# Kernel tuning notes

Hardware: AMD Instinct MI355X
Metric: run time of the kernel (lower is better)

## Reference

```python
import jax, jax.numpy as jnp
import numpy as np

B, P, N, L, H = 8, 1024, 32, 125, 256
E = 3 + L  # embed_dim = 3 local coords + latent_dim
OUTPUT_BIAS = 0.5   # cfg.supervision != 'sdf'
LEVEL_SET = -0.07   # cfg.level_set
SOFT_SCALE = 100.0  # cfg.soft_transfer_scale


def setup_inputs() -> dict:
    key = jax.random.key(0)
    ks = jax.random.split(key, 12)
    rn = lambda k, s, sc=1.0: jax.random.normal(k, s, dtype=jnp.float32) * sc
    X = rn(ks[0], (B, P, 3))
    latents = rn(ks[1], (N, B, L))
    constants = jax.random.uniform(ks[2], (B, N), minval=0.5, maxval=1.5, dtype=jnp.float32)
    scales = jax.random.uniform(ks[3], (B, N, 3), minval=0.5, maxval=1.5, dtype=jnp.float32)
    rotations = rn(ks[4], (B, N, 3, 3))
    centers = rn(ks[5], (B, N, 3))
    W0 = rn(ks[6], (N, E, H), 1.0 / np.sqrt(E))
    W1 = rn(ks[7], (N, H, H), 1.0 / np.sqrt(H))
    W2 = rn(ks[8], (N, H, H), 1.0 / np.sqrt(H))
    Wout = rn(ks[9], (N, H, 1), 1.0 / np.sqrt(H))
    return dict(X=X, latents=latents, constants=constants, scales=scales,
                rotations=rotations, centers=centers,
                W0=W0, b0=jnp.zeros((N, H), jnp.float32),
                W1=W1, b1=jnp.zeros((N, H), jnp.float32),
                W2=W2, b2=jnp.zeros((N, H), jnp.float32),
                Wout=Wout, bout=jnp.zeros((N, 1), jnp.float32),
                use_constants=1)


def _forward(X, latents, constants, scales, rotations, centers,
             W0, b0, W1, b1, W2, b2, Wout, bout, use_constants):
    b, p, _ = X.shape
    n, _, l = latents.shape
    # global_to_local: rotate (X - center) into each node frame, divide by scale
    diff = X[:, :, None, :] - centers[:, None]                      # [B,P,N,3]
    local = jnp.einsum('bnij,bpnj->bpni', rotations, diff) / scales[:, None]
    # concat local coords with per-node latent broadcast over points
    lat = jnp.broadcast_to(latents.transpose(1, 0, 2)[:, None], (b, p, n, l))
    inp = jnp.concatenate([local, lat], axis=-1)                    # [B,P,N,E]
    # per-node MLP stack as batched (grouped) GEMMs over the node axis
    h = jax.nn.relu(jnp.einsum('bpne,neh->bpnh', inp, W0) + b0)
    h = jax.nn.relu(jnp.einsum('bpnh,nhk->bpnk', h, W1) + b1)
    h = jax.nn.relu(jnp.einsum('bpnh,nhk->bpnk', h, W2) + b2)
    pred_sdf = jnp.einsum('bpnh,nho->bpno', h, Wout) + bout + OUTPUT_BIAS  # [B,P,N,1]
    # sample_rbf_weights: anisotropic gaussian weight per node
    w = jnp.exp(-0.5 * jnp.sum(local * local, axis=-1))             # [B,P,N]
    if use_constants:
        w = w * constants[:, None, :]
    w = w[..., None]                                                # [B,P,N,1]
    weighted_points_sdf = w * pred_sdf
    ldif_values = jnp.sum(weighted_points_sdf, axis=2)              # [B,P,1]
    # compute_inverse_occupancy: sigmoid(soft_scale * (level_set - values))
    class_pred = jax.nn.sigmoid(SOFT_SCALE * (LEVEL_SET - ldif_values))
    return ldif_values, class_pred


def reference(X, latents, constants, scales, rotations, centers,
              W0, b0, W1, b1, W2, b2, Wout, bout, use_constants):
    return _forward(X, latents, constants, scales, rotations, centers,
                    W0, b0, W1, b1, W2, b2, Wout, bout, use_constants)
```

## Files before the change

### kernel.cpp

```cpp
#include <hip/hip_runtime.h>
#include <math.h>

#define B_ 8
#define P_ 1024
#define N_ 32
#define L_ 125
#define H_ 256
#define E_ 128
#define MT 64

static_assert(E_ == 3 + L_, "embed dim mismatch");

typedef _Float16 half8 __attribute__((ext_vector_type(8)));
typedef _Float16 half4v __attribute__((ext_vector_type(4)));
typedef float f32x16 __attribute__((ext_vector_type(16)));

__global__ void prep(const float* __restrict__ latents,
                     const float* __restrict__ W0,
                     const float* __restrict__ b0,
                     const float* __restrict__ W1,
                     const float* __restrict__ W2,
                     float* __restrict__ Z,
                     _Float16* __restrict__ WThi,
                     _Float16* __restrict__ WTlo) {
  const int bid = blockIdx.x;
  const int t = threadIdx.x;
  if (bid < N_ * B_) {
    __shared__ float lat[L_];
    const int n = bid >> 3, b = bid & 7;
    if (t < L_) lat[t] = latents[(n * B_ + b) * L_ + t];
    __syncthreads();
    const float* w0 = W0 + ((size_t)n * E_ + 3) * H_ + t;
    float acc = b0[n * H_ + t];
#pragma unroll 5
    for (int l = 0; l < L_; ++l)
      acc = fmaf(lat[l], w0[(size_t)l * H_], acc);
    Z[(b * N_ + n) * H_ + t] = acc;
  } else {
    const int id = bid - N_ * B_;
    const int node = id >> 5;
    const int layer = (id >> 4) & 1;
    const int jb = (id >> 2) & 3;
    const int kb = id & 3;
    const float* W = (layer == 0 ? W1 : W2) + (size_t)node * H_ * H_;
    _Float16* dhi = WThi + ((size_t)layer * N_ + node) * H_ * H_;
    _Float16* dlo = WTlo + ((size_t)layer * N_ + node) * H_ * H_;
    __shared__ float tile[64][65];
    {
      const int col = t & 63;
#pragma unroll
      for (int i = 0; i < 16; ++i) {
        const int row = (t >> 6) * 16 + i;
        tile[row][col] = W[(size_t)(kb * 64 + row) * H_ + jb * 64 + col];
      }
    }
    __syncthreads();
    const int j_l = t >> 2;
    const int j = jb * 64 + j_l;
    const int w = j >> 5, lc = j & 31;
    const int kq = (t & 3) * 16;
    const int kc = kb * 4 + (t & 3);
    half8 hv0, hv1, lv0, lv1;
#pragma unroll
    for (int q = 0; q < 16; ++q) {
      const float v = tile[kq + q][j_l];
      const _Float16 hh = (_Float16)v;
      const _Float16 ll = (_Float16)(v - (float)hh);
      if (q < 8) { hv0[q] = hh; lv0[q] = ll; }
      else       { hv1[q - 8] = hh; lv1[q - 8] = ll; }
    }
    const size_t o0 = (size_t)w * 8192 + (size_t)kc * 512 + lc * 8;
    const size_t o1 = o0 + 256;
    *(half8*)(dhi + o0) = hv0;
    *(half8*)(dhi + o1) = hv1;
    *(half8*)(dlo + o0) = lv0;
    *(half8*)(dlo + o1) = lv1;
  }
}

__global__ __launch_bounds__(512, 2)
void mlp_main(const float* __restrict__ X,
              const float* __restrict__ constants,
              const float* __restrict__ scales,
              const float* __restrict__ rotations,
              const float* __restrict__ centers,
              const float* __restrict__ W0,
              const float* __restrict__ b1,
              const float* __restrict__ b2,
              const float* __restrict__ Wout,
              const float* __restrict__ bout,
              const float* __restrict__ Z,
              const _Float16* __restrict__ WThi,
              const _Float16* __restrict__ WTlo,
              const int* __restrict__ use_constants,
              float* __restrict__ pred) {
  __shared__ _Float16 h_hi[MT * H_];
  __shared__ _Float16 h_lo[MT * H_];
  __shared__ float loc[MT][3];
  __shared__ float wgt[MT];
  __shared__ float predpart[MT];

  const int ell = blockIdx.x;
  const int node = (ell & 7) * 4 + ((ell >> 3) & 3);
  const int p0 = (ell >> 5) * MT;
  const int b = p0 >> 10;
  const int tid = threadIdx.x;
  const int lane = tid & 63;
  const int w = tid >> 6;
  const int lc = lane & 31;
  const int kh = lane >> 5;

  if (tid < MT) {
    predpart[tid] = 0.f;
    const int pidx = p0 + tid;
    const float x0 = X[pidx * 3 + 0];
    const float x1 = X[pidx * 3 + 1];
    const float x2 = X[pidx * 3 + 2];
    const float* R = rotations + (size_t)(b * N_ + node) * 9;
    const float* C = centers + (size_t)(b * N_ + node) * 3;
    const float* S = scales + (size_t)(b * N_ + node) * 3;
    const float d0 = x0 - C[0], d1 = x1 - C[1], d2 = x2 - C[2];
    const float l0 = (R[0] * d0 + R[1] * d1 + R[2] * d2) / S[0];
    const float l1 = (R[3] * d0 + R[4] * d1 + R[5] * d2) / S[1];
    const float l2 = (R[6] * d0 + R[7] * d1 + R[8] * d2) / S[2];
    loc[tid][0] = l0; loc[tid][1] = l1; loc[tid][2] = l2;
    float ww = expf(-0.5f * (l0 * l0 + l1 * l1 + l2 * l2));
    if (use_constants[0] != 0) ww *= constants[b * N_ + node];
    wgt[tid] = ww;
  }
  __syncthreads();

  {
    const int m = lane;
    const float l0 = loc[m][0], l1 = loc[m][1], l2 = loc[m][2];
    const float* w0p = W0 + (size_t)node * E_ * H_;
    const float* zp = Z + (size_t)(b * N_ + node) * H_;
    char* hhp = (char*)h_hi + m * 512;
    char* hlp = (char*)h_lo + m * 512;
    const int mx = m & 31;
#pragma unroll
    for (int j = w * 32; j < w * 32 + 32; j += 4) {
      const float4 a0 = *(const float4*)(w0p + j);
      const float4 a1 = *(const float4*)(w0p + H_ + j);
      const float4 a2 = *(const float4*)(w0p + 2 * H_ + j);
      const float4 zz = *(const float4*)(zp + j);
      float v[4];
      v[0] = fmaxf(fmaf(l2, a2.x, fmaf(l1, a1.x, fmaf(l0, a0.x, zz.x))), 0.f);
      v[1] = fmaxf(fmaf(l2, a2.y, fmaf(l1, a1.y, fmaf(l0, a0.y, zz.y))), 0.f);
      v[2] = fmaxf(fmaf(l2, a2.z, fmaf(l1, a1.z, fmaf(l0, a0.z, zz.z))), 0.f);
      v[3] = fmaxf(fmaf(l2, a2.w, fmaf(l1, a1.w, fmaf(l0, a0.w, zz.w))), 0.f);
      half4v hv, lv;
#pragma unroll
      for (int r = 0; r < 4; ++r) {
        const _Float16 h16 = (_Float16)v[r];
        hv[r] = h16;
        lv[r] = (_Float16)(v[r] - (float)h16);
      }
      const int off = (((j >> 3) ^ mx) << 4) + ((j & 7) << 1);
      *(half4v*)(hhp + off) = hv;
      *(half4v*)(hlp + off) = lv;
    }
  }
  __syncthreads();

  f32x16 acc0, acc1;

  const size_t wb = (size_t)node * H_ * H_ + (size_t)w * 8192 + (kh * 32 + lc) * 8;
  const _Float16* wt1hi = WThi + wb;
  const _Float16* wt1lo = WTlo + wb;
  const _Float16* wt2hi = WThi + (size_t)N_ * H_ * H_ + wb;
  const _Float16* wt2lo = WTlo + (size_t)N_ * H_ * H_ + wb;

  const char* rbh0 = (const char*)h_hi + lc * 512;
  const char* rbh1 = (const char*)h_hi + (32 + lc) * 512;
  const char* rbl0 = (const char*)h_lo + lc * 512;
  const char* rbl1 = (const char*)h_lo + (32 + lc) * 512;

#define LDA(AH, AL, K) \
  AH = *(const half8*)(wh + (K) * 512); \
  AL = *(const half8*)(wl + (K) * 512);
#define LDB(B0, B1, B2, B3, K) { \
  const int so_ = ((2 * (K) + kh) ^ lc) << 4; \
  B0 = *(const half8*)(rbh0 + so_); \
  B1 = *(const half8*)(rbh1 + so_); \
  B2 = *(const half8*)(rbl0 + so_); \
  B3 = *(const half8*)(rbl1 + so_); }
#define MM(AH, AL, B0, B1, B2, B3) \
  __builtin_amdgcn_s_setprio(1); \
  acc0 = __builtin_amdgcn_mfma_f32_32x32x16_f16(AH, B0, acc0, 0, 0, 0); \
  acc1 = __builtin_amdgcn_mfma_f32_32x32x16_f16(AH, B1, acc1, 0, 0, 0); \
  acc0 = __builtin_amdgcn_mfma_f32_32x32x16_f16(AH, B2, acc0, 0, 0, 0); \
  acc1 = __builtin_amdgcn_mfma_f32_32x32x16_f16(AH, B3, acc1, 0, 0, 0); \
  acc0 = __builtin_amdgcn_mfma_f32_32x32x16_f16(AL, B0, acc0, 0, 0, 0); \
  acc1 = __builtin_amdgcn_mfma_f32_32x32x16_f16(AL, B1, acc1, 0, 0, 0); \
  __builtin_amdgcn_s_setprio(0);

  auto run_layer = [&](const _Float16* __restrict__ wh,
                       const _Float16* __restrict__ wl) {
    acc0 = (f32x16)(0.f);
    acc1 = (f32x16)(0.f);
    half8 A0H, A0L, A1H, A1L, A2H, A2L;
    half8 S0B0, S0B1, S0B2, S0B3, S1B0, S1B1, S1B2, S1B3;
    LDA(A0H, A0L, 0)
    LDA(A1H, A1L, 1)
    LDB(S0B0, S0B1, S0B2, S0B3, 0)
    LDA(A2H, A2L, 2)  LDB(S1B0, S1B1, S1B2, S1B3, 1)  MM(A0H, A0L, S0B0, S0B1, S0B2, S0B3)
    LDA(A0H, A0L, 3)  LDB(S0B0, S0B1, S0B2, S0B3, 2)  MM(A1H, A1L, S1B0, S1B1, S1B2, S1B3)
    LDA(A1H, A1L, 4)  LDB(S1B0, S1B1, S1B2, S1B3, 3)  MM(A2H, A2L, S0B0, S0B1, S0B2, S0B3)
    LDA(A2H, A2L, 5)  LDB(S0B0, S0B1, S0B2, S0B3, 4)  MM(A0H, A0L, S1B0, S1B1, S1B2, S1B3)
    LDA(A0H, A0L, 6)  LDB(S1B0, S1B1, S1B2, S1B3, 5)  MM(A1H, A1L, S0B0, S0B1, S0B2, S0B3)
    LDA(A1H, A1L, 7)  LDB(S0B0, S0B1, S0B2, S0B3, 6)  MM(A2H, A2L, S1B0, S1B1, S1B2, S1B3)
    LDA(A2H, A2L, 8)  LDB(S1B0, S1B1, S1B2, S1B3, 7)  MM(A0H, A0L, S0B0, S0B1, S0B2, S0B3)
    LDA(A0H, A0L, 9)  LDB(S0B0, S0B1, S0B2, S0B3, 8)  MM(A1H, A1L, S1B0, S1B1, S1B2, S1B3)
    LDA(A1H, A1L, 10) LDB(S1B0, S1B1, S1B2, S1B3, 9)  MM(A2H, A2L, S0B0, S0B1, S0B2, S0B3)
    LDA(A2H, A2L, 11) LDB(S0B0, S0B1, S0B2, S0B3, 10) MM(A0H, A0L, S1B0, S1B1, S1B2, S1B3)
    LDA(A0H, A0L, 12) LDB(S1B0, S1B1, S1B2, S1B3, 11) MM(A1H, A1L, S0B0, S0B1, S0B2, S0B3)
    LDA(A1H, A1L, 13) LDB(S0B0, S0B1, S0B2, S0B3, 12) MM(A2H, A2L, S1B0, S1B1, S1B2, S1B3)
    LDA(A2H, A2L, 14) LDB(S1B0, S1B1, S1B2, S1B3, 13) MM(A0H, A0L, S0B0, S0B1, S0B2, S0B3)
    LDA(A0H, A0L, 15) LDB(S0B0, S0B1, S0B2, S0B3, 14) MM(A1H, A1L, S1B0, S1B1, S1B2, S1B3)
                      LDB(S1B0, S1B1, S1B2, S1B3, 15) MM(A2H, A2L, S0B0, S0B1, S0B2, S0B3)
                                                      MM(A0H, A0L, S1B0, S1B1, S1B2, S1B3)
  };

  run_layer(wt1hi, wt1lo);
  __syncthreads();
  {
#pragma unroll
    for (int q = 0; q < 4; ++q) {
      const int jq = 32 * w + 8 * q + 4 * kh;
      const float4 bb = *(const float4*)(b1 + node * H_ + jq);
      const float bv[4] = {bb.x, bb.y, bb.z, bb.w};
      const int soff = ((((4 * w + q) ^ lc) << 4) + (kh << 3));
      half4v hv, lv;
#pragma unroll
      for (int r = 0; r < 4; ++r) {
        const float v = fmaxf(acc0[4 * q + r] + bv[r], 0.f);
        const _Float16 h16 = (_Float16)v;
        hv[r] = h16;
        lv[r] = (_Float16)(v - (float)h16);
      }
      *(half4v*)((char*)h_hi + lc * 512 + soff) = hv;
      *(half4v*)((char*)h_lo + lc * 512 + soff) = lv;
#pragma unroll
      for (int r = 0; r < 4; ++r) {
        const float v = fmaxf(acc1[4 * q + r] + bv[r], 0.f);
        const _Float16 h16 = (_Float16)v;
        hv[r] = h16;
        lv[r] = (_Float16)(v - (float)h16);
      }
      *(half4v*)((char*)h_hi + (32 + lc) * 512 + soff) = hv;
      *(half4v*)((char*)h_lo + (32 + lc) * 512 + soff) = lv;
    }
  }
  __syncthreads();

  run_layer(wt2hi, wt2lo);
  {
    float s0 = 0.f, s1 = 0.f;
#pragma unroll
    for (int q = 0; q < 4; ++q) {
      const int jq = 32 * w + 8 * q + 4 * kh;
      const float4 bb = *(const float4*)(b2 + node * H_ + jq);
      const float4 wo = *(const float4*)(Wout + node * H_ + jq);
      const float bv[4] = {bb.x, bb.y, bb.z, bb.w};
      const float wv[4] = {wo.x, wo.y, wo.z, wo.w};
#pragma unroll
      for (int r = 0; r < 4; ++r) {
        s0 = fmaf(fmaxf(acc0[4 * q + r] + bv[r], 0.f), wv[r], s0);
        s1 = fmaf(fmaxf(acc1[4 * q + r] + bv[r], 0.f), wv[r], s1);
      }
    }
    s0 += __shfl_xor(s0, 32, 64);
    s1 += __shfl_xor(s1, 32, 64);
    if (lane < 32) {
      atomicAdd(&predpart[lc], s0);
      atomicAdd(&predpart[32 + lc], s1);
    }
  }
  __syncthreads();

  if (tid < MT)
    pred[(size_t)node * (B_ * P_) + p0 + tid] =
        wgt[tid] * (predpart[tid] + bout[node] + 0.5f);
}

__global__ void finalize(const float* __restrict__ pred, float* __restrict__ out) {
  const int i = blockIdx.x * 256 + threadIdx.x;
  float v = 0.f;
#pragma unroll
  for (int n = 0; n < N_; ++n) v += pred[n * (B_ * P_) + i];
  out[i] = v;
  const float zz = 100.0f * (-0.07f - v);
  out[B_ * P_ + i] = 1.0f / (1.0f + expf(-zz));
}

extern "C" void kernel_launch(void* const* d_in, const int* in_sizes, int n_in,
                              void* d_out, int out_size, void* d_ws, size_t ws_size,
                              hipStream_t stream) {
  const float* X = (const float*)d_in[0];
  const float* latents = (const float*)d_in[1];
  const float* constants = (const float*)d_in[2];
  const float* scales = (const float*)d_in[3];
  const float* rotations = (const float*)d_in[4];
  const float* centers = (const float*)d_in[5];
  const float* W0 = (const float*)d_in[6];
  const float* b0 = (const float*)d_in[7];
  const float* W1 = (const float*)d_in[8];
  const float* b1 = (const float*)d_in[9];
  const float* W2 = (const float*)d_in[10];
  const float* b2 = (const float*)d_in[11];
  const float* Wout = (const float*)d_in[12];
  const float* bout = (const float*)d_in[13];
  const int* use_constants = (const int*)d_in[14];

  float* pred = (float*)d_ws;
  float* Zbuf = pred + (size_t)N_ * B_ * P_;
  _Float16* WThi = (_Float16*)(Zbuf + B_ * N_ * H_);
  _Float16* WTlo = WThi + (size_t)2 * N_ * H_ * H_;

  prep<<<dim3(N_ * B_ + N_ * 2 * 16), 256, 0, stream>>>(
      latents, W0, b0, W1, W2, Zbuf, WThi, WTlo);

  mlp_main<<<dim3(B_ * P_ / MT * N_), 512, 0, stream>>>(
      X, constants, scales, rotations, centers, W0, b1, b2, Wout, bout,
      Zbuf, WThi, WTlo, use_constants, pred);

  finalize<<<dim3(B_ * P_ / 256), 256, 0, stream>>>(pred, (float*)d_out);
}
```

Baseline: 322.7 us.

## Halve block to 4 waves, each computing two 32-column output tiles

The MLP kernel drops from 8 to 4 waves per block. Each wave now keeps four 32x32 accumulators and covers two column groups, so every B fragment read from LDS feeds twice as many MFMAs and LDS read traffic per FLOP goes down. The first-layer fill loop is widened so that 256 threads still cover all 64 rows by 256 columns. The cost is more accumulator and A-fragment registers per wave, plus a launch bound of 4 blocks per CU, which may limit occupancy or cause spills.

```diff
diff --git a/kernel.cpp b/kernel.cpp
--- a/kernel.cpp
+++ b/kernel.cpp
@@ -57,7 +57,7 @@
     __syncthreads();
     const int j_l = t >> 2;
     const int j = jb * 64 + j_l;
-    const int w = j >> 5, lc = j & 31;
+    const int jg = j >> 5, lc = j & 31;
     const int kq = (t & 3) * 16;
     const int kc = kb * 4 + (t & 3);
     half8 hv0, hv1, lv0, lv1;
@@ -69,7 +69,7 @@
       if (q < 8) { hv0[q] = hh; lv0[q] = ll; }
       else       { hv1[q - 8] = hh; lv1[q - 8] = ll; }
     }
-    const size_t o0 = (size_t)w * 8192 + (size_t)kc * 512 + lc * 8;
+    const size_t o0 = (size_t)jg * 8192 + (size_t)kc * 512 + lc * 8;
     const size_t o1 = o0 + 256;
     *(half8*)(dhi + o0) = hv0;
     *(half8*)(dhi + o1) = hv1;
@@ -78,7 +78,7 @@
   }
 }
 
-__global__ __launch_bounds__(512, 2)
+__global__ __launch_bounds__(256, 4)
 void mlp_main(const float* __restrict__ X,
               const float* __restrict__ constants,
               const float* __restrict__ scales,
@@ -131,7 +131,8 @@
   __syncthreads();
 
   {
-    const int m = lane;
+    const int m = tid & 63;
+    const int jr = (tid >> 6) * 64;
     const float l0 = loc[m][0], l1 = loc[m][1], l2 = loc[m][2];
     const float* w0p = W0 + (size_t)node * E_ * H_;
     const float* zp = Z + (size_t)(b * N_ + node) * H_;
@@ -139,7 +140,7 @@
     char* hlp = (char*)h_lo + m * 512;
     const int mx = m & 31;
 #pragma unroll
-    for (int j = w * 32; j < w * 32 + 32; j += 4) {
+    for (int j = jr; j < jr + 64; j += 4) {
       const float4 a0 = *(const float4*)(w0p + j);
       const float4 a1 = *(const float4*)(w0p + H_ + j);
       const float4 a2 = *(const float4*)(w0p + 2 * H_ + j);
@@ -163,9 +164,9 @@
   }
   __syncthreads();
 
-  f32x16 acc0, acc1;
-
-  const size_t wb = (size_t)node * H_ * H_ + (size_t)w * 8192 + (kh * 32 + lc) * 8;
+  f32x16 acc00, acc01, acc10, acc11;
+
+  const size_t wb = (size_t)node * H_ * H_ + (size_t)(2 * w) * 8192 + (kh * 32 + lc) * 8;
   const _Float16* wt1hi = WThi + wb;
   const _Float16* wt1lo = WTlo + wb;
   const _Float16* wt2hi = WThi + (size_t)N_ * H_ * H_ + wb;
@@ -176,80 +177,92 @@
   const char* rbl0 = (const char*)h_lo + lc * 512;
   const char* rbl1 = (const char*)h_lo + (32 + lc) * 512;
 
-#define LDA(AH, AL, K) \
-  AH = *(const half8*)(wh + (K) * 512); \
-  AL = *(const half8*)(wl + (K) * 512);
+#define LDA(H0, L0, H1, L1, K) \
+  H0 = *(const half8*)(wh + (K) * 512); \
+  L0 = *(const half8*)(wl + (K) * 512); \
+  H1 = *(const half8*)(wh + 8192 + (K) * 512); \
+  L1 = *(const half8*)(wl + 8192 + (K) * 512);
 #define LDB(B0, B1, B2, B3, K) { \
   const int so_ = ((2 * (K) + kh) ^ lc) << 4; \
   B0 = *(const half8*)(rbh0 + so_); \
   B1 = *(const half8*)(rbh1 + so_); \
   B2 = *(const half8*)(rbl0 + so_); \
   B3 = *(const half8*)(rbl1 + so_); }
-#define MM(AH, AL, B0, B1, B2, B3) \
+#define MM(H0, L0, H1, L1, B0, B1, B2, B3) \
   __builtin_amdgcn_s_setprio(1); \
-  acc0 = __builtin_amdgcn_mfma_f32_32x32x16_f16(AH, B0, acc0, 0, 0, 0); \
-  acc1 = __builtin_amdgcn_mfma_f32_32x32x16_f16(AH, B1, acc1, 0, 0, 0); \
-  acc0 = __builtin_amdgcn_mfma_f32_32x32x16_f16(AH, B2, acc0, 0, 0, 0); \
-  acc1 = __builtin_amdgcn_mfma_f32_32x32x16_f16(AH, B3, acc1, 0, 0, 0); \
-  acc0 = __builtin_amdgcn_mfma_f32_32x32x16_f16(AL, B0, acc0, 0, 0, 0); \
-  acc1 = __builtin_amdgcn_mfma_f32_32x32x16_f16(AL, B1, acc1, 0, 0, 0); \
+  acc00 = __builtin_amdgcn_mfma_f32_32x32x16_f16(H0, B0, acc00, 0, 0, 0); \
+  acc01 = __builtin_amdgcn_mfma_f32_32x32x16_f16(H0, B1, acc01, 0, 0, 0); \
+  acc10 = __builtin_amdgcn_mfma_f32_32x32x16_f16(H1, B0, acc10, 0, 0, 0); \
+  acc11 = __builtin_amdgcn_mfma_f32_32x32x16_f16(H1, B1, acc11, 0, 0, 0); \
+  acc00 = __builtin_amdgcn_mfma_f32_32x32x16_f16(H0, B2, acc00, 0, 0, 0); \
+  acc01 = __builtin_amdgcn_mfma_f32_32x32x16_f16(H0, B3, acc01, 0, 0, 0); \
+  acc10 = __builtin_amdgcn_mfma_f32_32x32x16_f16(H1, B2, acc10, 0, 0, 0); \
+  acc11 = __builtin_amdgcn_mfma_f32_32x32x16_f16(H1, B3, acc11, 0, 0, 0); \
+  acc00 = __builtin_amdgcn_mfma_f32_32x32x16_f16(L0, B0, acc00, 0, 0, 0); \
+  acc01 = __builtin_amdgcn_mfma_f32_32x32x16_f16(L0, B1, acc01, 0, 0, 0); \
+  acc10 = __builtin_amdgcn_mfma_f32_32x32x16_f16(L1, B0, acc10, 0, 0, 0); \
+  acc11 = __builtin_amdgcn_mfma_f32_32x32x16_f16(L1, B1, acc11, 0, 0, 0); \
   __builtin_amdgcn_s_setprio(0);
 
   auto run_layer = [&](const _Float16* __restrict__ wh,
                        const _Float16* __restrict__ wl) {
-    acc0 = (f32x16)(0.f);
-    acc1 = (f32x16)(0.f);
-    half8 A0H, A0L, A1H, A1L, A2H, A2L;
+    acc00 = (f32x16)(0.f);
+    acc01 = (f32x16)(0.f);
+    acc10 = (f32x16)(0.f);
+    acc11 = (f32x16)(0.f);
+    half8 A0H0, A0L0, A0H1, A0L1, A1H0, A1L0, A1H1, A1L1;
     half8 S0B0, S0B1, S0B2, S0B3, S1B0, S1B1, S1B2, S1B3;
-    LDA(A0H, A0L, 0)
-    LDA(A1H, A1L, 1)
+    LDA(A0H0, A0L0, A0H1, A0L1, 0)
     LDB(S0B0, S0B1, S0B2, S0B3, 0)
-    LDA(A2H, A2L, 2)  LDB(S1B0, S1B1, S1B2, S1B3, 1)  MM(A0H, A0L, S0B0, S0B1, S0B2, S0B3)
-    LDA(A0H, A0L, 3)  LDB(S0B0, S0B1, S0B2, S0B3, 2)  MM(A1H, A1L, S1B0, S1B1, S1B2, S1B3)
-    LDA(A1H, A1L, 4)  LDB(S1B0, S1B1, S1B2, S1B3, 3)  MM(A2H, A2L, S0B0, S0B1, S0B2, S0B3)
-    LDA(A2H, A2L, 5)  LDB(S0B0, S0B1, S0B2, S0B3, 4)  MM(A0H, A0L, S1B0, S1B1, S1B2, S1B3)
-    LDA(A0H, A0L, 6)  LDB(S1B0, S1B1, S1B2, S1B3, 5)  MM(A1H, A1L, S0B0, S0B1, S0B2, S0B3)
-    LDA(A1H, A1L, 7)  LDB(S0B0, S0B1, S0B2, S0B3, 6)  MM(A2H, A2L, S1B0, S1B1, S1B2, S1B3)
-    LDA(A2H, A2L, 8)  LDB(S1B0, S1B1, S1B2, S1B3, 7)  MM(A0H, A0L, S0B0, S0B1, S0B2, S0B3)
-    LDA(A0H, A0L, 9)  LDB(S0B0, S0B1, S0B2, S0B3, 8)  MM(A1H, A1L, S1B0, S1B1, S1B2, S1B3)
-    LDA(A1H, A1L, 10) LDB(S1B0, S1B1, S1B2, S1B3, 9)  MM(A2H, A2L, S0B0, S0B1, S0B2, S0B3)
-    LDA(A2H, A2L, 11) LDB(S0B0, S0B1, S0B2, S0B3, 10) MM(A0H, A0L, S1B0, S1B1, S1B2, S1B3)
-    LDA(A0H, A0L, 12) LDB(S1B0, S1B1, S1B2, S1B3, 11) MM(A1H, A1L, S0B0, S0B1, S0B2, S0B3)
-    LDA(A1H, A1L, 13) LDB(S0B0, S0B1, S0B2, S0B3, 12) MM(A2H, A2L, S1B0, S1B1, S1B2, S1B3)
-    LDA(A2H, A2L, 14) LDB(S1B0, S1B1, S1B2, S1B3, 13) MM(A0H, A0L, S0B0, S0B1, S0B2, S0B3)
-    LDA(A0H, A0L, 15) LDB(S0B0, S0B1, S0B2, S0B3, 14) MM(A1H, A1L, S1B0, S1B1, S1B2, S1B3)
-                      LDB(S1B0, S1B1, S1B2, S1B3, 15) MM(A2H, A2L, S0B0, S0B1, S0B2, S0B3)
-                                                      MM(A0H, A0L, S1B0, S1B1, S1B2, S1B3)
+    LDA(A1H0, A1L0, A1H1, A1L1, 1)  LDB(S1B0, S1B1, S1B2, S1B3, 1)  MM(A0H0, A0L0, A0H1, A0L1, S0B0, S0B1, S0B2, S0B3)
+    LDA(A0H0, A0L0, A0H1, A0L1, 2)  LDB(S0B0, S0B1, S0B2, S0B3, 2)  MM(A1H0, A1L0, A1H1, A1L1, S1B0, S1B1, S1B2, S1B3)
+    LDA(A1H0, A1L0, A1H1, A1L1, 3)  LDB(S1B0, S1B1, S1B2, S1B3, 3)  MM(A0H0, A0L0, A0H1, A0L1, S0B0, S0B1, S0B2, S0B3)
+    LDA(A0H0, A0L0, A0H1, A0L1, 4)  LDB(S0B0, S0B1, S0B2, S0B3, 4)  MM(A1H0, A1L0, A1H1, A1L1, S1B0, S1B1, S1B2, S1B3)
+    LDA(A1H0, A1L0, A1H1, A1L1, 5)  LDB(S1B0, S1B1, S1B2, S1B3, 5)  MM(A0H0, A0L0, A0H1, A0L1, S0B0, S0B1, S0B2, S0B3)
+    LDA(A0H0, A0L0, A0H1, A0L1, 6)  LDB(S0B0, S0B1, S0B2, S0B3, 6)  MM(A1H0, A1L0, A1H1, A1L1, S1B0, S1B1, S1B2, S1B3)
+    LDA(A1H0, A1L0, A1H1, A1L1, 7)  LDB(S1B0, S1B1, S1B2, S1B3, 7)  MM(A0H0, A0L0, A0H1, A0L1, S0B0, S0B1, S0B2, S0B3)
+    LDA(A0H0, A0L0, A0H1, A0L1, 8)  LDB(S0B0, S0B1, S0B2, S0B3, 8)  MM(A1H0, A1L0, A1H1, A1L1, S1B0, S1B1, S1B2, S1B3)
+    LDA(A1H0, A1L0, A1H1, A1L1, 9)  LDB(S1B0, S1B1, S1B2, S1B3, 9)  MM(A0H0, A0L0, A0H1, A0L1, S0B0, S0B1, S0B2, S0B3)
+    LDA(A0H0, A0L0, A0H1, A0L1, 10) LDB(S0B0, S0B1, S0B2, S0B3, 10) MM(A1H0, A1L0, A1H1, A1L1, S1B0, S1B1, S1B2, S1B3)
+    LDA(A1H0, A1L0, A1H1, A1L1, 11) LDB(S1B0, S1B1, S1B2, S1B3, 11) MM(A0H0, A0L0, A0H1, A0L1, S0B0, S0B1, S0B2, S0B3)
+    LDA(A0H0, A0L0, A0H1, A0L1, 12) LDB(S0B0, S0B1, S0B2, S0B3, 12) MM(A1H0, A1L0, A1H1, A1L1, S1B0, S1B1, S1B2, S1B3)
+    LDA(A1H0, A1L0, A1H1, A1L1, 13) LDB(S1B0, S1B1, S1B2, S1B3, 13) MM(A0H0, A0L0, A0H1, A0L1, S0B0, S0B1, S0B2, S0B3)
+    LDA(A0H0, A0L0, A0H1, A0L1, 14) LDB(S0B0, S0B1, S0B2, S0B3, 14) MM(A1H0, A1L0, A1H1, A1L1, S1B0, S1B1, S1B2, S1B3)
+    LDA(A1H0, A1L0, A1H1, A1L1, 15) LDB(S1B0, S1B1, S1B2, S1B3, 15) MM(A0H0, A0L0, A0H1, A0L1, S0B0, S0B1, S0B2, S0B3)
+                                                                    MM(A1H0, A1L0, A1H1, A1L1, S1B0, S1B1, S1B2, S1B3)
   };
 
   run_layer(wt1hi, wt1lo);
   __syncthreads();
   {
 #pragma unroll
-    for (int q = 0; q < 4; ++q) {
-      const int jq = 32 * w + 8 * q + 4 * kh;
-      const float4 bb = *(const float4*)(b1 + node * H_ + jq);
-      const float bv[4] = {bb.x, bb.y, bb.z, bb.w};
-      const int soff = ((((4 * w + q) ^ lc) << 4) + (kh << 3));
-      half4v hv, lv;
-#pragma unroll
-      for (int r = 0; r < 4; ++r) {
-        const float v = fmaxf(acc0[4 * q + r] + bv[r], 0.f);
-        const _Float16 h16 = (_Float16)v;
-        hv[r] = h16;
-        lv[r] = (_Float16)(v - (float)h16);
+    for (int jt = 0; jt < 2; ++jt) {
+#pragma unroll
+      for (int q = 0; q < 4; ++q) {
+        const int jq = 64 * w + 32 * jt + 8 * q + 4 * kh;
+        const float4 bb = *(const float4*)(b1 + node * H_ + jq);
+        const float bv[4] = {bb.x, bb.y, bb.z, bb.w};
+        const int soff = ((((8 * w + 4 * jt + q) ^ lc) << 4) + (kh << 3));
+        half4v hv, lv;
+#pragma unroll
+        for (int r = 0; r < 4; ++r) {
+          const float v = fmaxf((jt == 0 ? acc00[4 * q + r] : acc10[4 * q + r]) + bv[r], 0.f);
+          const _Float16 h16 = (_Float16)v;
+          hv[r] = h16;
+          lv[r] = (_Float16)(v - (float)h16);
+        }
+        *(half4v*)((char*)h_hi + lc * 512 + soff) = hv;
+        *(half4v*)((char*)h_lo + lc * 512 + soff) = lv;
+#pragma unroll
+        for (int r = 0; r < 4; ++r) {
+          const float v = fmaxf((jt == 0 ? acc01[4 * q + r] : acc11[4 * q + r]) + bv[r], 0.f);
+          const _Float16 h16 = (_Float16)v;
+          hv[r] = h16;
+          lv[r] = (_Float16)(v - (float)h16);
+        }
+        *(half4v*)((char*)h_hi + (32 + lc) * 512 + soff) = hv;
+        *(half4v*)((char*)h_lo + (32 + lc) * 512 + soff) = lv;
       }
-      *(half4v*)((char*)h_hi + lc * 512 + soff) = hv;
-      *(half4v*)((char*)h_lo + lc * 512 + soff) = lv;
-#pragma unroll
-      for (int r = 0; r < 4; ++r) {
-        const float v = fmaxf(acc1[4 * q + r] + bv[r], 0.f);
-        const _Float16 h16 = (_Float16)v;
-        hv[r] = h16;
-        lv[r] = (_Float16)(v - (float)h16);
-      }
-      *(half4v*)((char*)h_hi + (32 + lc) * 512 + soff) = hv;
-      *(half4v*)((char*)h_lo + (32 + lc) * 512 + soff) = lv;
     }
   }
   __syncthreads();
@@ -258,16 +271,21 @@
   {
     float s0 = 0.f, s1 = 0.f;
 #pragma unroll
-    for (int q = 0; q < 4; ++q) {
-      const int jq = 32 * w + 8 * q + 4 * kh;
-      const float4 bb = *(const float4*)(b2 + node * H_ + jq);
-      const float4 wo = *(const float4*)(Wout + node * H_ + jq);
-      const float bv[4] = {bb.x, bb.y, bb.z, bb.w};
-      const float wv[4] = {wo.x, wo.y, wo.z, wo.w};
-#pragma unroll
-      for (int r = 0; r < 4; ++r) {
-        s0 = fmaf(fmaxf(acc0[4 * q + r] + bv[r], 0.f), wv[r], s0);
-        s1 = fmaf(fmaxf(acc1[4 * q + r] + bv[r], 0.f), wv[r], s1);
+    for (int jt = 0; jt < 2; ++jt) {
+#pragma unroll
+      for (int q = 0; q < 4; ++q) {
+        const int jq = 64 * w + 32 * jt + 8 * q + 4 * kh;
+        const float4 bb = *(const float4*)(b2 + node * H_ + jq);
+        const float4 wo = *(const float4*)(Wout + node * H_ + jq);
+        const float bv[4] = {bb.x, bb.y, bb.z, bb.w};
+        const float wv[4] = {wo.x, wo.y, wo.z, wo.w};
+#pragma unroll
+        for (int r = 0; r < 4; ++r) {
+          const float a0v = (jt == 0 ? acc00[4 * q + r] : acc10[4 * q + r]);
+          const float a1v = (jt == 0 ? acc01[4 * q + r] : acc11[4 * q + r]);
+          s0 = fmaf(fmaxf(a0v + bv[r], 0.f), wv[r], s0);
+          s1 = fmaf(fmaxf(a1v + bv[r], 0.f), wv[r], s1);
+        }
       }
     }
     s0 += __shfl_xor(s0, 32, 64);
@@ -321,7 +339,7 @@
   prep<<<dim3(N_ * B_ + N_ * 2 * 16), 256, 0, stream>>>(
       latents, W0, b0, W1, W2, Zbuf, WThi, WTlo);
 
-  mlp_main<<<dim3(B_ * P_ / MT * N_), 512, 0, stream>>>(
+  mlp_main<<<dim3(B_ * P_ / MT * N_), 256, 0, stream>>>(
       X, constants, scales, rotations, centers, W0, b1, b2, Wout, bout,
       Zbuf, WThi, WTlo, use_constants, pred);
 
```

New measurement: 288.6 us. -10.6%, faster.
